# Performance work log

Measured on AMD Instinct MI355X. Metric: run time of the kernel, lower is better.

The kernel has to match this reference:

```python
import jax, jax.numpy as jnp
import numpy as np

NUM_HEADS = 12

def _get_rel_pos(size, rel_pos):
    # q_size == k_size == size, no interpolation needed (table has 2*size-1 rows)
    idx = jnp.arange(size)[:, None] - jnp.arange(size)[None, :] + (size - 1)  # (size,size)
    return rel_pos[idx]  # (size, size, head_dim)

def setup_inputs() -> dict:
    key = jax.random.key(0)
    ks = jax.random.split(key, 7)
    B, H, W, dim = 8, 32, 32, 768
    head_dim = dim // NUM_HEADS
    return {
        "x": jax.random.normal(ks[0], (B, H, W, dim), jnp.float32),
        "qkv_w": jax.random.normal(ks[1], (dim, 3 * dim), jnp.float32) * 0.02,
        "qkv_b": jax.random.normal(ks[2], (3 * dim,), jnp.float32) * 0.02,
        "proj_w": jax.random.normal(ks[3], (dim, dim), jnp.float32) * 0.02,
        "proj_b": jax.random.normal(ks[4], (dim,), jnp.float32) * 0.02,
        "rel_pos_h": jax.random.normal(ks[5], (2 * H - 1, head_dim), jnp.float32) * 0.02,
        "rel_pos_w": jax.random.normal(ks[6], (2 * W - 1, head_dim), jnp.float32) * 0.02,
    }

def reference(x, qkv_w, qkv_b, proj_w, proj_b, rel_pos_h, rel_pos_w):
    B, H, W, dim = x.shape
    N = H * W
    head_dim = dim // NUM_HEADS
    scale = head_dim ** (-0.5)

    qkv = x.reshape(B, N, dim) @ qkv_w + qkv_b                     # (B,N,3*dim)
    qkv = qkv.reshape(B, N, 3, NUM_HEADS, head_dim)
    qkv = qkv.transpose(2, 0, 3, 1, 4).reshape(3, B * NUM_HEADS, N, head_dim)
    q, k, v = qkv[0], qkv[1], qkv[2]                               # (B*h, N, hd)

    attn = jnp.einsum("bnd,bmd->bnm", q * scale, k)                # (B*h, N, N)

    # decomposed relative position bias
    Rh = _get_rel_pos(H, rel_pos_h)                                # (H,H,hd)
    Rw = _get_rel_pos(W, rel_pos_w)                                # (W,W,hd)
    r_q = q.reshape(B * NUM_HEADS, H, W, head_dim)
    rel_h = jnp.einsum("bhwc,hkc->bhwk", r_q, Rh)                  # (B*h,H,W,H)
    rel_w = jnp.einsum("bhwc,wkc->bhwk", r_q, Rw)                  # (B*h,H,W,W)
    attn = (attn.reshape(B * NUM_HEADS, H, W, H, W)
            + rel_h[:, :, :, :, None]
            + rel_w[:, :, :, None, :]).reshape(B * NUM_HEADS, N, N)

    attn = jax.nn.softmax(attn, axis=-1)
    out = jnp.einsum("bnm,bmd->bnd", attn, v)                      # (B*h, N, hd)
    out = out.reshape(B, NUM_HEADS, H, W, head_dim).transpose(0, 2, 3, 1, 4).reshape(B, H, W, dim)
    return out @ proj_w + proj_b
```

## Files before the change

kernel.cpp:

```cpp
#include <hip/hip_runtime.h>
#include <hip/hip_bf16.h>
#include <math.h>

#define DIM   768
#define NHEAD 12
#define NQ    1024

typedef short  short8  __attribute__((ext_vector_type(8)));
typedef unsigned short us8 __attribute__((ext_vector_type(8)));
typedef float  f32x16  __attribute__((ext_vector_type(16)));

#if __has_builtin(__builtin_amdgcn_exp2f)
#define EXP2(x) __builtin_amdgcn_exp2f(x)
#else
#define EXP2(x) __expf(0.69314718056f * (x))
#endif
#define LOG2E 1.44269504089f

__device__ inline ushort f2b(float f) {
  union { float f; unsigned u; } c; c.f = f;
  unsigned r = (c.u + 0x7FFFu + ((c.u >> 16) & 1u)) >> 16;
  return (ushort)r;
}
__device__ inline float b2f(ushort h) {
  union { unsigned u; float f; } c; c.u = ((unsigned)h) << 16;
  return c.f;
}
__device__ inline ushort4 cvt4(float4 v) {
  ushort4 o; o.x = f2b(v.x); o.y = f2b(v.y); o.z = f2b(v.z); o.w = f2b(v.w);
  return o;
}
__device__ inline unsigned pkr(float a, float b) {
  union { float f; unsigned u; } ca, cb; ca.f = a; cb.f = b;
  return __builtin_amdgcn_perm(cb.u + 0x8000u, ca.u + 0x8000u, 0x07060302u);
}
__device__ __forceinline__ void gload16(const void* g, void* l) {
  __builtin_amdgcn_global_load_lds(
      (const __attribute__((address_space(1))) void*)g,
      (__attribute__((address_space(3))) void*)l, 16, 0, 0);
}

__global__ __launch_bounds__(256) void prep(
    const float* __restrict__ x, const float* __restrict__ qkv_w,
    const float* __restrict__ proj_w, ushort* __restrict__ Xb,
    ushort* __restrict__ Wqt, ushort* __restrict__ Wpt) {
  __shared__ ushort Ts[64][68];
  const int blk = blockIdx.x, tid = threadIdx.x;
  if (blk < 768) {
    const float4* src = (const float4*)x;
    ushort4* dst = (ushort4*)Xb;
    int base = blk * 2048;
#pragma unroll
    for (int it = 0; it < 8; ++it) {
      int i = base + it * 256 + tid;
      dst[i] = cvt4(src[i]);
    }
    return;
  }
  const float* W; ushort* Wt; int ncols, tk, tn;
  if (blk < 1200) { int t = blk - 768;  W = qkv_w; Wt = Wqt; ncols = 2304; tk = t % 12; tn = t / 12; }
  else            { int t = blk - 1200; W = proj_w; Wt = Wpt; ncols = 768; tk = t % 12; tn = t / 12; }
  const int kb = tk * 64, nb = tn * 64;
#pragma unroll
  for (int rr = 0; rr < 4; ++rr) {
    int r = (tid >> 4) + rr * 16, c4 = (tid & 15) * 4;
    float4 w = *(const float4*)(W + (size_t)(kb + r) * ncols + nb + c4);
    *(ushort4*)&Ts[r][c4] = cvt4(w);
  }
  __syncthreads();
#pragma unroll
  for (int wwi = 0; wwi < 2; ++wwi) {
    int n = (tid >> 3) + wwi * 32, k8 = (tid & 7) * 8;
    us8 v;
#pragma unroll
    for (int j = 0; j < 8; ++j) v[j] = Ts[k8 + j][n];
    *(us8*)(Wt + (size_t)(nb + n) * 768 + kb + k8) = v;
  }
}

template <int OUTBF>
__global__ __launch_bounds__(256, 4) void gemm_mfma(
    const ushort* __restrict__ A, const ushort* __restrict__ BT,
    const float* __restrict__ bias, void* __restrict__ Cp, int Nc,
    ushort* __restrict__ VTg) {
  __shared__ __align__(16) ushort As[128 * 64];
  __shared__ __align__(16) ushort Bs[128 * 64];
  const int tid = threadIdx.x;
  const int bm = blockIdx.y * 128, bn = blockIdx.x * 128;
  const int lane = tid & 63, wv = tid >> 6;
  const int l31 = lane & 31, lh = lane >> 5;
  const int wm = (wv >> 1) * 64, wn = (wv & 1) * 64;
  const int xr = l31 & 7;

  const int dr = lane >> 3;
  const int ccol = ((lane & 7) ^ dr) * 8;
  const ushort* ag = A + (size_t)(bm + wv * 32 + dr) * 768 + ccol;
  const ushort* bg = BT + (size_t)(bn + wv * 32 + dr) * 768 + ccol;
  ushort* al = &As[wv * 32 * 64];
  ushort* bl = &Bs[wv * 32 * 64];

  f32x16 acc[2][2];
#pragma unroll
  for (int i = 0; i < 2; ++i)
#pragma unroll
    for (int j = 0; j < 2; ++j)
#pragma unroll
      for (int r = 0; r < 16; ++r) acc[i][j][r] = 0.f;

  for (int kt = 0; kt < 768; kt += 64) {
    __syncthreads();
#pragma unroll
    for (int wi = 0; wi < 4; ++wi) {
      gload16(ag + kt + wi * (8 * 768), al + wi * 512);
      gload16(bg + kt + wi * (8 * 768), bl + wi * 512);
    }
    __syncthreads();
#pragma unroll
    for (int ks = 0; ks < 4; ++ks) {
      const int ca = ((ks * 2 + lh) ^ xr) * 8;
      short8 a0 = *(const short8*)&As[(wm + l31) * 64 + ca];
      short8 a1 = *(const short8*)&As[(wm + 32 + l31) * 64 + ca];
      short8 b0 = *(const short8*)&Bs[(wn + l31) * 64 + ca];
      short8 b1 = *(const short8*)&Bs[(wn + 32 + l31) * 64 + ca];
      acc[0][0] = __builtin_amdgcn_mfma_f32_32x32x16_bf16(a0, b0, acc[0][0], 0, 0, 0);
      acc[0][1] = __builtin_amdgcn_mfma_f32_32x32x16_bf16(a0, b1, acc[0][1], 0, 0, 0);
      acc[1][0] = __builtin_amdgcn_mfma_f32_32x32x16_bf16(a1, b0, acc[1][0], 0, 0, 0);
      acc[1][1] = __builtin_amdgcn_mfma_f32_32x32x16_bf16(a1, b1, acc[1][1], 0, 0, 0);
    }
  }

  const bool vreg = OUTBF && (bn >= 1536);
  if (!vreg) {
#pragma unroll
    for (int mb = 0; mb < 2; ++mb)
#pragma unroll
      for (int nb = 0; nb < 2; ++nb) {
        int col = bn + wn + nb * 32 + l31;
        float bv = bias[col];
#pragma unroll
        for (int reg = 0; reg < 16; ++reg) {
          int row = bm + wm + mb * 32 + (reg & 3) + 8 * (reg >> 2) + 4 * lh;
          float o = acc[mb][nb][reg] + bv;
          if (OUTBF) ((ushort*)Cp)[(size_t)row * Nc + col] = f2b(o);
          else       ((float*)Cp)[(size_t)row * Nc + col] = o;
        }
      }
  } else {
    const int b_ = bm >> 10;
    const int nbase = (bm & 1023) + wm;
#pragma unroll
    for (int nb = 0; nb < 2; ++nb) {
      int col = bn + wn + nb * 32 + l31;
      float bv = bias[col];
      int hd_ = col - 1536;
      int h_ = hd_ >> 6, d_ = hd_ & 63;
      ushort* vrow = VTg + ((size_t)(b_ * NHEAD + h_) * 64 + d_) * NQ;
#pragma unroll
      for (int mb = 0; mb < 2; ++mb)
#pragma unroll
        for (int g = 0; g < 4; ++g) {
          int n = nbase + mb * 32 + 8 * g + 4 * lh;
          ushort4 st;
          st.x = f2b(acc[mb][nb][4 * g + 0] + bv);
          st.y = f2b(acc[mb][nb][4 * g + 1] + bv);
          st.z = f2b(acc[mb][nb][4 * g + 2] + bv);
          st.w = f2b(acc[mb][nb][4 * g + 3] + bv);
          *(ushort4*)(vrow + n) = st;
        }
    }
  }
}

__global__ __launch_bounds__(256, 4) void attn_mfma(
    const ushort* __restrict__ QKV, const ushort* __restrict__ VTg,
    const float* __restrict__ rph, const float* __restrict__ rpw,
    ushort* __restrict__ O) {
  __shared__ ushort Qs[128][72];
  __shared__ __align__(16) ushort KV[2 * 64 * 64];

  ushort* const Ksp = KV;
  ushort* const VTp = KV + 64 * 64;

  const int tid = threadIdx.x;
  const int bh = blockIdx.x % 96;
  const int qt = blockIdx.x / 96;
  const int b = bh / NHEAD, h = bh % NHEAD;
  const int n0 = qt * 128;
  const int lane = tid & 63, wv = tid >> 6;
  const int l31 = lane & 31, lh = lane >> 5;
  const int wb = wv * 32;
  const int xr = l31 & 7;

  const ushort* qb = QKV + (size_t)b * NQ * 2304 + h * 64;
  const ushort* kb = qb + DIM;
  const ushort* vtg = VTg + (size_t)bh * 64 * NQ;

#pragma unroll
  for (int it = 0; it < 4; ++it) {
    int item = tid + 256 * it;
    int r = item >> 3, c8 = (item & 7) * 8;
    *(us8*)&Qs[r][c8] = *(const us8*)(qb + (size_t)(n0 + r) * 2304 + c8);
  }
#pragma unroll
  for (int it = 0; it < 4; ++it) {
    int item = tid + 256 * it;
    int r = item >> 4, c4 = (item & 15) * 4;
    if (r < 63) {
      float4 vh = *(const float4*)(rph + r * 64 + c4);
      vh.x *= LOG2E; vh.y *= LOG2E; vh.z *= LOG2E; vh.w *= LOG2E;
      *(ushort4*)&Ksp[r * 64 + c4] = cvt4(vh);
      float4 vw = *(const float4*)(rpw + r * 64 + c4);
      vw.x *= LOG2E; vw.y *= LOG2E; vw.z *= LOG2E; vw.w *= LOG2E;
      *(ushort4*)&VTp[r * 64 + c4] = cvt4(vw);
    } else {
      ushort4 z = {0, 0, 0, 0};
      *(ushort4*)&Ksp[r * 64 + c4] = z;
      *(ushort4*)&VTp[r * 64 + c4] = z;
    }
  }

  const int dr = lane >> 3;
  const int ccol = ((lane & 7) ^ dr) * 8;
  const ushort* kg = kb + (size_t)(wv * 16 + dr) * 2304 + ccol;
  const ushort* vg = vtg + (size_t)(wv * 16 + dr) * NQ + ccol;
  ushort* kl = &Ksp[wv * 16 * 64];
  ushort* vl = &VTp[wv * 16 * 64];

  __syncthreads();

  short8 aq[4];
#pragma unroll
  for (int ks = 0; ks < 4; ++ks)
    aq[ks] = *(const short8*)&Qs[wb + l31][ks * 16 + lh * 8];

  __syncthreads();

  ushort* Pb2 = &Qs[0][0] + wv * (32 * 40);
  ushort* rhs = &Qs[0][0] + 5120;

  {
    const int hq31 = qt * 4 + wv + 31;
    f32x16 sh;
#pragma unroll
    for (int i = 0; i < 16; ++i) sh[i] = 0.f;
#pragma unroll
    for (int ks = 0; ks < 4; ++ks) {
      short8 at = *(const short8*)&Ksp[(hq31 - l31) * 64 + ks * 16 + lh * 8];
      sh = __builtin_amdgcn_mfma_f32_32x32x16_bf16(at, aq[ks], sh, 0, 0, 0);
    }
#pragma unroll
    for (int reg = 0; reg < 16; ++reg) {
      int hk = (reg & 3) + 8 * (reg >> 2) + 4 * lh;
      rhs[hk * 128 + wb + l31] = f2b(sh[reg]);
    }
  }

  float rwv[16];
  {
    short8 at[8];
#pragma unroll
    for (int ub = 0; ub < 2; ++ub)
#pragma unroll
      for (int ks = 0; ks < 4; ++ks)
        at[ub * 4 + ks] =
            *(const short8*)&VTp[(ub * 32 + l31) * 64 + ks * 16 + lh * 8];
    f32x16 su0, su1;
#pragma unroll
    for (int i = 0; i < 16; ++i) { su0[i] = 0.f; su1[i] = 0.f; }
#pragma unroll
    for (int ks = 0; ks < 4; ++ks) {
      su0 = __builtin_amdgcn_mfma_f32_32x32x16_bf16(at[ks],     aq[ks], su0, 0, 0, 0);
      su1 = __builtin_amdgcn_mfma_f32_32x32x16_bf16(at[4 + ks], aq[ks], su1, 0, 0, 0);
    }
    __syncthreads();
#pragma unroll
    for (int reg = 0; reg < 16; ++reg) {
      int rm = (reg & 3) + 8 * (reg >> 2) + 4 * lh;
      KV[rm * 128 + wb + l31]        = f2b(su0[reg]);
      KV[(32 + rm) * 128 + wb + l31] = f2b(su1[reg]);
    }
#pragma unroll
    for (int reg = 0; reg < 16; ++reg) {
      int rm = (reg & 3) + 8 * (reg >> 2) + 4 * lh;
      rwv[reg] = b2f(KV[(31 + l31 - rm) * 128 + wb + l31]);
    }
  }

  f32x16 oacc0, oacc1;
#pragma unroll
  for (int i = 0; i < 16; ++i) { oacc0[i] = 0.f; oacc1[i] = 0.f; }
  float lacc = 0.f;

  for (int t = 0; t < 16; ++t) {
    const int kt = t * 64;
    __syncthreads();
    gload16(kg + (size_t)kt * 2304,              kl);
    gload16(kg + (size_t)kt * 2304 + 8 * 2304,   kl + 512);
    gload16(vg + kt,                             vl);
    gload16(vg + kt + 8 * NQ,                    vl + 512);
    __syncthreads();

    const float rh0 = b2f(rhs[(2 * t) * 128 + wb + l31]);
    const float rh1 = b2f(rhs[(2 * t + 1) * 128 + wb + l31]);

#pragma unroll
    for (int cb = 0; cb < 2; ++cb) {
      f32x16 s;
#pragma unroll
      for (int i = 0; i < 16; ++i) s[i] = 0.f;
#pragma unroll
      for (int ks = 0; ks < 4; ++ks) {
        const int ck = ((ks * 2 + lh) ^ xr) * 8;
        short8 ak = *(const short8*)&Ksp[(cb * 32 + l31) * 64 + ck];
        s = __builtin_amdgcn_mfma_f32_32x32x16_bf16(ak, aq[ks], s, 0, 0, 0);
      }
      const float rhv = cb ? rh1 : rh0;
#pragma unroll
      for (int g = 0; g < 4; ++g) {
        float p0 = EXP2(fmaf(s[4 * g + 0], 0.18033688f, rwv[4 * g + 0] + rhv));
        float p1 = EXP2(fmaf(s[4 * g + 1], 0.18033688f, rwv[4 * g + 1] + rhv));
        float p2 = EXP2(fmaf(s[4 * g + 2], 0.18033688f, rwv[4 * g + 2] + rhv));
        float p3 = EXP2(fmaf(s[4 * g + 3], 0.18033688f, rwv[4 * g + 3] + rhv));
        lacc += (p0 + p1) + (p2 + p3);
        uint2 pk; pk.x = pkr(p0, p1); pk.y = pkr(p2, p3);
        *(uint2*)&Pb2[l31 * 40 + 8 * g + 4 * lh] = pk;
      }
#pragma unroll
      for (int ks = 0; ks < 2; ++ks) {
        const int cv = ((cb * 4 + ks * 2 + lh) ^ xr) * 8;
        short8 ap  = *(const short8*)&Pb2[l31 * 40 + ks * 16 + lh * 8];
        short8 bv0 = *(const short8*)&VTp[l31 * 64 + cv];
        short8 bv1 = *(const short8*)&VTp[(32 + l31) * 64 + cv];
        oacc0 = __builtin_amdgcn_mfma_f32_32x32x16_bf16(ap, bv0, oacc0, 0, 0, 0);
        oacc1 = __builtin_amdgcn_mfma_f32_32x32x16_bf16(ap, bv1, oacc1, 0, 0, 0);
      }
    }
  }

  lacc += __shfl_xor(lacc, 32);
  const float linv = 1.0f / lacc;
  ushort* ob = O + ((size_t)b * NQ + n0 + wb) * DIM + h * 64;
#pragma unroll
  for (int reg = 0; reg < 16; ++reg) {
    int row = (reg & 3) + 8 * (reg >> 2) + 4 * lh;
    float lq = __shfl(linv, row);
    ob[(size_t)row * DIM + l31]      = f2b(oacc0[reg] * lq);
    ob[(size_t)row * DIM + 32 + l31] = f2b(oacc1[reg] * lq);
  }
}

extern "C" void kernel_launch(void* const* d_in, const int* in_sizes, int n_in,
                              void* d_out, int out_size, void* d_ws, size_t ws_size,
                              hipStream_t stream) {
  const float* x      = (const float*)d_in[0];
  const float* qkv_w  = (const float*)d_in[1];
  const float* qkv_b  = (const float*)d_in[2];
  const float* proj_w = (const float*)d_in[3];
  const float* proj_b = (const float*)d_in[4];
  const float* rel_h  = (const float*)d_in[5];
  const float* rel_w  = (const float*)d_in[6];
  float* out = (float*)d_out;

  ushort* qkvb = (ushort*)d_ws;
  ushort* obuf = qkvb + (size_t)8192 * 2304;
  ushort* Xb   = obuf + (size_t)8192 * DIM;
  ushort* Wqt  = Xb + (size_t)8192 * DIM;
  ushort* Wpt  = Wqt + (size_t)2304 * DIM;
  ushort* VTg  = Wpt + (size_t)DIM * DIM;

  prep<<<dim3(1344), 256, 0, stream>>>(x, qkv_w, proj_w, Xb, Wqt, Wpt);

  gemm_mfma<1><<<dim3(2304 / 128, 8192 / 128), 256, 0, stream>>>(
      Xb, Wqt, qkv_b, qkvb, 2304, VTg);

  attn_mfma<<<dim3(96 * 8), 256, 0, stream>>>(qkvb, VTg, rel_h, rel_w, obuf);

  gemm_mfma<0><<<dim3(768 / 128, 8192 / 128), 256, 0, stream>>>(
      obuf, Wpt, proj_b, out, 768, nullptr);
}
```

Baseline: 206.9 us.

## Split GEMM into QKV and projection kernels with swizzled block order

The templated GEMM is split into a QKV-specific kernel and a projection-specific kernel. Both now use a 1D grid remapped so that consecutive blocks land on different XCD-interleaved row groups, which is meant to improve L2 reuse of the A/B tiles. The projection GEMM moves to a 128x64 tile so the grid grows from 384 to 768 blocks, which raises occupancy on the 256-CU device. The cost is less reuse per block and a smaller MFMA count per load in the projection kernel.

```diff
diff --git a/kernel.cpp b/kernel.cpp
--- a/kernel.cpp
+++ b/kernel.cpp
@@ -78,15 +78,18 @@
   }
 }
 
-template <int OUTBF>
-__global__ __launch_bounds__(256, 4) void gemm_mfma(
+__global__ __launch_bounds__(256, 4) void gemm_qkv(
     const ushort* __restrict__ A, const ushort* __restrict__ BT,
-    const float* __restrict__ bias, void* __restrict__ Cp, int Nc,
+    const float* __restrict__ bias, ushort* __restrict__ Cp,
     ushort* __restrict__ VTg) {
   __shared__ __align__(16) ushort As[128 * 64];
   __shared__ __align__(16) ushort Bs[128 * 64];
   const int tid = threadIdx.x;
-  const int bm = blockIdx.y * 128, bn = blockIdx.x * 128;
+  const int flat = blockIdx.x;
+  const int g = flat >> 3;
+  const int by = (flat & 7) * 8 + g / 18;
+  const int bx = g % 18;
+  const int bm = by * 128, bn = bx * 128;
   const int lane = tid & 63, wv = tid >> 6;
   const int l31 = lane & 31, lh = lane >> 5;
   const int wm = (wv >> 1) * 64, wn = (wv & 1) * 64;
@@ -129,8 +132,7 @@
     }
   }
 
-  const bool vreg = OUTBF && (bn >= 1536);
-  if (!vreg) {
+  if (bn < 1536) {
 #pragma unroll
     for (int mb = 0; mb < 2; ++mb)
 #pragma unroll
@@ -140,9 +142,7 @@
 #pragma unroll
         for (int reg = 0; reg < 16; ++reg) {
           int row = bm + wm + mb * 32 + (reg & 3) + 8 * (reg >> 2) + 4 * lh;
-          float o = acc[mb][nb][reg] + bv;
-          if (OUTBF) ((ushort*)Cp)[(size_t)row * Nc + col] = f2b(o);
-          else       ((float*)Cp)[(size_t)row * Nc + col] = o;
+          Cp[(size_t)row * 2304 + col] = f2b(acc[mb][nb][reg] + bv);
         }
       }
   } else {
@@ -158,16 +158,72 @@
 #pragma unroll
       for (int mb = 0; mb < 2; ++mb)
 #pragma unroll
-        for (int g = 0; g < 4; ++g) {
-          int n = nbase + mb * 32 + 8 * g + 4 * lh;
+        for (int g2 = 0; g2 < 4; ++g2) {
+          int n = nbase + mb * 32 + 8 * g2 + 4 * lh;
           ushort4 st;
-          st.x = f2b(acc[mb][nb][4 * g + 0] + bv);
-          st.y = f2b(acc[mb][nb][4 * g + 1] + bv);
-          st.z = f2b(acc[mb][nb][4 * g + 2] + bv);
-          st.w = f2b(acc[mb][nb][4 * g + 3] + bv);
+          st.x = f2b(acc[mb][nb][4 * g2 + 0] + bv);
+          st.y = f2b(acc[mb][nb][4 * g2 + 1] + bv);
+          st.z = f2b(acc[mb][nb][4 * g2 + 2] + bv);
+          st.w = f2b(acc[mb][nb][4 * g2 + 3] + bv);
           *(ushort4*)(vrow + n) = st;
         }
     }
+  }
+}
+
+__global__ __launch_bounds__(256, 4) void gemm_proj(
+    const ushort* __restrict__ A, const ushort* __restrict__ BT,
+    const float* __restrict__ bias, float* __restrict__ C) {
+  __shared__ __align__(16) ushort As[128 * 64];
+  __shared__ __align__(16) ushort Bs[64 * 64];
+  const int tid = threadIdx.x;
+  const int flat = blockIdx.x;
+  const int g = flat >> 3;
+  const int by = (flat & 7) * 8 + g / 12;
+  const int bx = g % 12;
+  const int bm = by * 128, bn = bx * 64;
+  const int lane = tid & 63, wv = tid >> 6;
+  const int l31 = lane & 31, lh = lane >> 5;
+  const int wm = (wv >> 1) * 64, wn = (wv & 1) * 32;
+  const int xr = l31 & 7;
+
+  const int dr = lane >> 3;
+  const int ccol = ((lane & 7) ^ dr) * 8;
+  const ushort* ag = A + (size_t)(bm + wv * 32 + dr) * 768 + ccol;
+  const ushort* bg = BT + (size_t)(bn + wv * 16 + dr) * 768 + ccol;
+  ushort* al = &As[wv * 32 * 64];
+  ushort* bl = &Bs[wv * 16 * 64];
+
+  f32x16 acc0, acc1;
+#pragma unroll
+  for (int r = 0; r < 16; ++r) { acc0[r] = 0.f; acc1[r] = 0.f; }
+
+  for (int kt = 0; kt < 768; kt += 64) {
+    __syncthreads();
+#pragma unroll
+    for (int wi = 0; wi < 4; ++wi)
+      gload16(ag + kt + wi * (8 * 768), al + wi * 512);
+    gload16(bg + kt,            bl);
+    gload16(bg + kt + 8 * 768,  bl + 512);
+    __syncthreads();
+#pragma unroll
+    for (int ks = 0; ks < 4; ++ks) {
+      const int ca = ((ks * 2 + lh) ^ xr) * 8;
+      short8 a0 = *(const short8*)&As[(wm + l31) * 64 + ca];
+      short8 a1 = *(const short8*)&As[(wm + 32 + l31) * 64 + ca];
+      short8 b0 = *(const short8*)&Bs[(wn + l31) * 64 + ca];
+      acc0 = __builtin_amdgcn_mfma_f32_32x32x16_bf16(a0, b0, acc0, 0, 0, 0);
+      acc1 = __builtin_amdgcn_mfma_f32_32x32x16_bf16(a1, b0, acc1, 0, 0, 0);
+    }
+  }
+
+  const int col = bn + wn + l31;
+  const float bv = bias[col];
+#pragma unroll
+  for (int reg = 0; reg < 16; ++reg) {
+    int row = bm + wm + (reg & 3) + 8 * (reg >> 2) + 4 * lh;
+    C[(size_t)row * 768 + col]        = acc0[reg] + bv;
+    C[(size_t)(row + 32) * 768 + col] = acc1[reg] + bv;
   }
 }
 
@@ -370,11 +426,9 @@
 
   prep<<<dim3(1344), 256, 0, stream>>>(x, qkv_w, proj_w, Xb, Wqt, Wpt);
 
-  gemm_mfma<1><<<dim3(2304 / 128, 8192 / 128), 256, 0, stream>>>(
-      Xb, Wqt, qkv_b, qkvb, 2304, VTg);
+  gemm_qkv<<<dim3(1152), 256, 0, stream>>>(Xb, Wqt, qkv_b, qkvb, VTg);
 
   attn_mfma<<<dim3(96 * 8), 256, 0, stream>>>(qkvb, VTg, rel_h, rel_w, obuf);
 
-  gemm_mfma<0><<<dim3(768 / 128, 8192 / 128), 256, 0, stream>>>(
-      obuf, Wpt, proj_b, out, 768, nullptr);
-}
+  gemm_proj<<<dim3(768), 256, 0, stream>>>(obuf, Wpt, proj_b, out);
+}
```

After: 192.6 us. 1.07x faster.
